# Performance work log

Hardware: AMD Instinct MI355X
Metric: run time of the kernel (lower is better)

## Reference

```python
import jax, jax.numpy as jnp
import numpy as np

B, S, D, H = 2, 2048, 768, 12
HD = D // H  # head dim = 64

def setup_inputs() -> dict:
    key = jax.random.key(0)
    ks = jax.random.split(key, 9)
    s = 1.0 / np.sqrt(D)
    return {
        "x": jax.random.normal(ks[0], (B, S, D), dtype=jnp.float32),
        "Wq": jax.random.uniform(ks[1], (D, D), jnp.float32, -s, s),
        "bq": jax.random.uniform(ks[2], (D,), jnp.float32, -s, s),
        "Wk": jax.random.uniform(ks[3], (D, D), jnp.float32, -s, s),
        "bk": jax.random.uniform(ks[4], (D,), jnp.float32, -s, s),
        "Wv": jax.random.uniform(ks[5], (D, D), jnp.float32, -s, s),
        "bv": jax.random.uniform(ks[6], (D,), jnp.float32, -s, s),
        "Wo": jax.random.uniform(ks[7], (D, D), jnp.float32, -s, s),
        "bo": jax.random.uniform(ks[8], (D,), jnp.float32, -s, s),
    }

def reference(x, Wq, bq, Wk, bk, Wv, bv, Wo, bo):
    b, s, _ = x.shape
    # linear projections, split into heads: [b, h, s, hd]
    def proj(W, bias):
        y = x @ W + bias
        return y.reshape(b, s, H, HD).transpose(0, 2, 1, 3)
    q = proj(Wq, bq)
    k = proj(Wk, bk)
    v = proj(Wv, bv)
    scale = 1.0 / np.sqrt(HD).astype(np.float32)
    scores = jnp.einsum('bhqd,bhkd->bhqk', q, k) * scale
    attn = jax.nn.softmax(scores, axis=-1)
    out = jnp.einsum('bhqk,bhkd->bhqd', attn, v)
    out = out.transpose(0, 2, 1, 3).reshape(b, s, D)
    return out @ Wo + bo
```

## Files before the change

### kernel.cpp

```cpp
#include <hip/hip_runtime.h>
#include <math.h>

#define NH 12
#define SEQ 2048
#define DM 768
#define HD 64
#define NB 2
#define MT (NB * SEQ)
#define QSCL 0.18033688011112042591999058512524f

typedef short bf16x8 __attribute__((ext_vector_type(8)));
typedef float f32x16 __attribute__((ext_vector_type(16)));

__device__ __forceinline__ unsigned short bf16_rne(float x) {
    unsigned u = __float_as_uint(x);
    u += 0x7fffu + ((u >> 16) & 1u);
    return (unsigned short)(u >> 16);
}
__device__ __forceinline__ float bf16_tof(short h) {
    return __uint_as_float(((unsigned)(unsigned short)h) << 16);
}

__device__ __forceinline__ void gl_lds16(const void* g, void* s) {
    __builtin_amdgcn_global_load_lds(
        (const __attribute__((address_space(1))) unsigned int*)g,
        (__attribute__((address_space(3))) unsigned int*)s, 16, 0, 0);
}

__device__ __forceinline__ f32x16 mfma32(bf16x8 a, bf16x8 b, f32x16 c) {
    return __builtin_amdgcn_mfma_f32_32x32x16_bf16(a, b, c, 0, 0, 0);
}

__device__ __forceinline__ bf16x8 gfrag(const char* base, int row, int physblk) {
    return *(const bf16x8*)(base + row * 64 + physblk * 16);
}
__device__ __forceinline__ bf16x8 afrag(const short* base, int row, int blk) {
    return *(const bf16x8*)(base + row * 64 + ((blk ^ (row & 7)) << 3));
}

__global__ __launch_bounds__(256)
void conv_x(const float* __restrict__ x, short* __restrict__ xg)
{
    const int idx = blockIdx.x * 256 + threadIdx.x;
    const int m = idx / 96, bk = idx % 96;
    const float* src = x + (size_t)m * DM + bk * 8;
    float4 v0 = *(const float4*)src;
    float4 v1 = *(const float4*)(src + 4);
    const float vv[8] = {v0.x, v0.y, v0.z, v0.w, v1.x, v1.y, v1.z, v1.w};
    union { short s[8]; int4 q; } hh;
#pragma unroll
    for (int j = 0; j < 8; j++) hh.s[j] = (short)bf16_rne(vv[j]);
    const int pb = (bk & ~3) | ((bk & 3) ^ ((m >> 1) & 3));
    *(int4*)(xg + (size_t)m * DM + pb * 8) = hh.q;
}

__global__ __launch_bounds__(256)
void conv_wt(const float* __restrict__ Wq, const float* __restrict__ Wk,
             const float* __restrict__ Wv, const float* __restrict__ Wo,
             short* __restrict__ wdst)
{
    const int z = blockIdx.y;
    const float* __restrict__ W = (z == 0) ? Wq : (z == 1) ? Wk : (z == 2) ? Wv : Wo;
    const int idx = blockIdx.x * 256 + threadIdx.x;
    const int n = idx % 768, bk = idx / 768;
    union { short s[8]; int4 q; } hh;
#pragma unroll
    for (int j = 0; j < 8; j++) hh.s[j] = (short)bf16_rne(W[(size_t)(bk * 8 + j) * DM + n]);
    const int pb = (bk & ~3) | ((bk & 3) ^ ((n >> 1) & 3));
    *(int4*)(wdst + (size_t)z * 589824 + (size_t)n * DM + pb * 8) = hh.q;
}

__global__ __launch_bounds__(256)
void gemm_qkv(const short* __restrict__ xg, const short* __restrict__ wt,
              const float* __restrict__ bq, const float* __restrict__ bkv,
              const float* __restrict__ bv,
              short* __restrict__ qg, short* __restrict__ kg, short* __restrict__ vg)
{
    const int z = blockIdx.z;
    const short* __restrict__ Bw = wt + (size_t)z * 589824;
    const float* __restrict__ bias = (z == 0) ? bq : (z == 1) ? bkv : bv;

    __shared__ short As[4096], Bs[4096];
    const int t = threadIdx.x, w = t >> 6, l = t & 63;
    const int by = blockIdx.y, bx = blockIdx.x;

    const int lr = w * 32 + (l >> 2);
    const char* pA = (const char*)xg + (size_t)(by * 128 + lr) * 1536 + (l & 3) * 16;
    const char* pB = (const char*)Bw + (size_t)(bx * 128 + lr) * 1536 + (l & 3) * 16;
    char* sA = (char*)As;
    char* sB = (char*)Bs;
    const int lo = w * 2048;

    const int mrow = (w >> 1) * 64 + (l & 31);
    const int nrow = (w & 1) * 64 + (l & 31);
    const int sel  = ((l & 31) >> 1) & 3;
    const int half = l >> 5;

    f32x16 acc[2][2];
#pragma unroll
    for (int i = 0; i < 2; i++)
#pragma unroll
        for (int j = 0; j < 2; j++)
#pragma unroll
            for (int r = 0; r < 16; r++) acc[i][j][r] = 0.f;

    for (int k0 = 0; k0 < DM; k0 += 32) {
        const size_t cb = (size_t)k0 * 2;
        __syncthreads();
#pragma unroll
        for (int i = 0; i < 2; i++) {
            gl_lds16(pA + i * 24576 + cb, sA + lo + i * 1024);
            gl_lds16(pB + i * 24576 + cb, sB + lo + i * 1024);
        }
        __syncthreads();
#pragma unroll
        for (int s = 0; s < 2; s++) {
            const int blk = s * 2 + half;
            bf16x8 a0 = gfrag(sA, mrow,      blk ^ sel);
            bf16x8 a1 = gfrag(sA, mrow + 32, blk ^ sel);
            bf16x8 b0 = gfrag(sB, nrow,      blk ^ sel);
            bf16x8 b1 = gfrag(sB, nrow + 32, blk ^ sel);
            acc[0][0] = mfma32(a0, b0, acc[0][0]);
            acc[0][1] = mfma32(a0, b1, acc[0][1]);
            acc[1][0] = mfma32(a1, b0, acc[1][0]);
            acc[1][1] = mfma32(a1, b1, acc[1][1]);
        }
    }

    const int mb = by * 128 + (w >> 1) * 64 + 4 * half;
    const int nb = bx * 128 + (w & 1) * 64 + (l & 31);

    if (z == 2) {
#pragma unroll
        for (int ti = 0; ti < 2; ti++)
#pragma unroll
            for (int g = 0; g < 4; g++)
#pragma unroll
                for (int tj = 0; tj < 2; tj++) {
                    const int m0 = mb + ti * 32 + 8 * g;
                    const int bb = m0 >> 11, ss = m0 & 2047;
                    const int n = nb + tj * 32;
                    const int h = n >> 6, hd = n & 63;
                    const float bia = bias[n];
                    union { unsigned short u[4]; uint2 q; } pk;
#pragma unroll
                    for (int j = 0; j < 4; j++)
                        pk.u[j] = bf16_rne(acc[ti][tj][4 * g + j] + bia);
                    const int blk = ss >> 3;
                    const int phys = (blk & ~7) | ((blk & 7) ^ (hd & 7));
                    *(uint2*)(vg + ((size_t)(bb * NH + h) * HD + hd) * SEQ + phys * 8 + (ss & 7)) = pk.q;
                }
    } else {
        short* dst = (z == 0) ? qg : kg;
        const float scl = (z == 0) ? QSCL : 1.0f;
#pragma unroll
        for (int ti = 0; ti < 2; ti++)
#pragma unroll
            for (int tj = 0; tj < 2; tj++) {
                const int n = nb + tj * 32;
                const int h = n >> 6, hd = n & 63;
                const float bia = bias[n];
                const int blk = hd >> 3;
#pragma unroll
                for (int r = 0; r < 16; r++) {
                    const int m = mb + ti * 32 + (r & 3) + 8 * (r >> 2);
                    const int bb = m >> 11, ss = m & 2047;
                    const int phys = blk ^ (ss & 7);
                    dst[((size_t)(bb * NH + h) * SEQ + ss) * HD + phys * 8 + (hd & 7)] =
                        (short)bf16_rne((acc[ti][tj][r] + bia) * scl);
                }
            }
    }
}

__global__ __launch_bounds__(256)
void attn_mfma(const short* __restrict__ qg, const short* __restrict__ kg,
               const short* __restrict__ vg,
               short* __restrict__ opart, float* __restrict__ lpart)
{
    __shared__ short Qs[8192];
    __shared__ short Ks[4096];
    __shared__ short Vt[4096];
    __shared__ short Ps[8192];

    const int t = threadIdx.x, w = t >> 6, l = t & 63;
    const int bh = blockIdx.y, q0 = blockIdx.x * 128, ks = blockIdx.z;
    const char* qp = (const char*)(qg + (size_t)bh * SEQ * HD);
    const char* kp = (const char*)(kg + (size_t)bh * SEQ * HD);
    const char* vp = (const char*)(vg + (size_t)bh * HD * SEQ);

#pragma unroll
    for (int i = 0; i < 4; i++)
        gl_lds16(qp + (size_t)(q0 + w * 32 + i * 8) * 128 + l * 16,
                 (char*)Qs + (w * 32 + i * 8) * 128);

    const int half = l >> 5;
    bf16x8 qf[4];
    f32x16 oacc[2], lacc;
#pragma unroll
    for (int nt = 0; nt < 2; nt++)
#pragma unroll
        for (int r = 0; r < 16; r++) oacc[nt][r] = 0.f;
#pragma unroll
    for (int r = 0; r < 16; r++) lacc[r] = 0.f;

    bf16x8 onesf;
#pragma unroll
    for (int j = 0; j < 8; j++) onesf[j] = (short)0x3F80;

    short* psw = Ps + w * 2048;

    for (int kti = 0; kti < 16; kti++) {
        const int kb0 = (ks * 16 + kti) * 64;
        __syncthreads();
#pragma unroll
        for (int i = 0; i < 2; i++) {
            gl_lds16(kp + (size_t)(kb0 + w * 16 + i * 8) * 128 + l * 16,
                     (char*)Ks + (w * 16 + i * 8) * 128);
            gl_lds16(vp + (size_t)(w * 16 + i * 8 + (l >> 3)) * 4096 + kb0 * 2 + (l & 7) * 16,
                     (char*)Vt + (w * 16 + i * 8) * 128);
        }
        __syncthreads();

        if (kti == 0) {
#pragma unroll
            for (int s = 0; s < 4; s++)
                qf[s] = afrag(Qs, w * 32 + (l & 31), half + s * 2);
        }

        f32x16 sacc[2];
#pragma unroll
        for (int nt = 0; nt < 2; nt++)
#pragma unroll
            for (int r = 0; r < 16; r++) sacc[nt][r] = 0.f;
#pragma unroll
        for (int s = 0; s < 4; s++) {
#pragma unroll
            for (int nt = 0; nt < 2; nt++) {
                bf16x8 kf = afrag(Ks, nt * 32 + (l & 31), half + s * 2);
                sacc[nt] = mfma32(qf[s], kf, sacc[nt]);
            }
        }

#pragma unroll
        for (int r = 0; r < 16; r++) {
            const int row = (r & 3) + 8 * (r >> 2) + 4 * half;
            const float p0 = exp2f(sacc[0][r]);
            const float p1 = exp2f(sacc[1][r]);
            const int b0 = (l & 31) >> 3;
            psw[row * 64 + ((b0 ^ (row & 7)) << 3) + (l & 7)]       = (short)bf16_rne(p0);
            psw[row * 64 + (((b0 + 4) ^ (row & 7)) << 3) + (l & 7)] = (short)bf16_rne(p1);
        }

#pragma unroll
        for (int s = 0; s < 4; s++) {
            bf16x8 pf = afrag(psw, l & 31, half + s * 2);
            lacc = mfma32(pf, onesf, lacc);
#pragma unroll
            for (int nt = 0; nt < 2; nt++) {
                bf16x8 vf = afrag(Vt, nt * 32 + (l & 31), half + s * 2);
                oacc[nt] = mfma32(pf, vf, oacc[nt]);
            }
        }
    }

    const size_t base = (size_t)(ks * 24 + bh) * SEQ;
#pragma unroll
    for (int r = 0; r < 16; r++) {
        const int row = q0 + w * 32 + (r & 3) + 8 * (r >> 2) + 4 * half;
#pragma unroll
        for (int nt = 0; nt < 2; nt++)
            opart[(base + row) * 64 + nt * 32 + (l & 31)] = (short)bf16_rne(oacc[nt][r]);
        if ((l & 31) == 0) lpart[base + row] = lacc[r];
    }
}

__global__ __launch_bounds__(256)
void attn_reduce(const short* __restrict__ opart, const float* __restrict__ lpart,
                 short* __restrict__ ag)
{
    const int idx = blockIdx.x * 256 + threadIdx.x;
    const int cg = idx & 7, row = idx >> 3;
    const int bh = row >> 11, s = row & 2047;
    union { short s[8]; int4 q; } a, b, o;
    a.q = *(const int4*)(opart + ((size_t)bh * SEQ + s) * 64 + cg * 8);
    b.q = *(const int4*)(opart + ((size_t)(24 + bh) * SEQ + s) * 64 + cg * 8);
    const float inv = 1.0f / (lpart[(size_t)bh * SEQ + s] + lpart[(size_t)(24 + bh) * SEQ + s]);
#pragma unroll
    for (int j = 0; j < 8; j++)
        o.s[j] = (short)bf16_rne((bf16_tof(a.s[j]) + bf16_tof(b.s[j])) * inv);
    const int bb = bh / NH, h = bh % NH;
    const int m = bb * SEQ + s;
    const int blk = h * 8 + cg;
    const int phys = (blk & ~3) | ((blk & 3) ^ ((m >> 1) & 3));
    *(int4*)(ag + (size_t)m * DM + phys * 8) = o.q;
}

__global__ __launch_bounds__(256)
void gemm_out(const short* __restrict__ ag, const short* __restrict__ wt3,
              const float* __restrict__ bias, float* __restrict__ out)
{
    __shared__ short As[4096], Bs[4096];
    const int t = threadIdx.x, w = t >> 6, l = t & 63;
    const int by = blockIdx.y, bx = blockIdx.x;

    const int lr = w * 32 + (l >> 2);
    const char* pA = (const char*)ag  + (size_t)(by * 128 + lr) * 1536 + (l & 3) * 16;
    const char* pB = (const char*)wt3 + (size_t)(bx * 128 + lr) * 1536 + (l & 3) * 16;
    char* sA = (char*)As;
    char* sB = (char*)Bs;
    const int lo = w * 2048;

    const int mrow = (w >> 1) * 64 + (l & 31);
    const int nrow = (w & 1) * 64 + (l & 31);
    const int sel  = ((l & 31) >> 1) & 3;
    const int half = l >> 5;

    f32x16 acc[2][2];
#pragma unroll
    for (int i = 0; i < 2; i++)
#pragma unroll
        for (int j = 0; j < 2; j++)
#pragma unroll
            for (int r = 0; r < 16; r++) acc[i][j][r] = 0.f;

    for (int k0 = 0; k0 < DM; k0 += 32) {
        const size_t cb = (size_t)k0 * 2;
        __syncthreads();
#pragma unroll
        for (int i = 0; i < 2; i++) {
            gl_lds16(pA + i * 24576 + cb, sA + lo + i * 1024);
            gl_lds16(pB + i * 24576 + cb, sB + lo + i * 1024);
        }
        __syncthreads();
#pragma unroll
        for (int s = 0; s < 2; s++) {
            const int blk = s * 2 + half;
            bf16x8 a0 = gfrag(sA, mrow,      blk ^ sel);
            bf16x8 a1 = gfrag(sA, mrow + 32, blk ^ sel);
            bf16x8 b0 = gfrag(sB, nrow,      blk ^ sel);
            bf16x8 b1 = gfrag(sB, nrow + 32, blk ^ sel);
            acc[0][0] = mfma32(a0, b0, acc[0][0]);
            acc[0][1] = mfma32(a0, b1, acc[0][1]);
            acc[1][0] = mfma32(a1, b0, acc[1][0]);
            acc[1][1] = mfma32(a1, b1, acc[1][1]);
        }
    }

    const int mb = by * 128 + (w >> 1) * 64 + 4 * half;
    const int nb = bx * 128 + (w & 1) * 64 + (l & 31);
#pragma unroll
    for (int ti = 0; ti < 2; ti++)
#pragma unroll
        for (int tj = 0; tj < 2; tj++) {
            const int n = nb + tj * 32;
            const float bia = bias[n];
#pragma unroll
            for (int r = 0; r < 16; r++) {
                const int m = mb + ti * 32 + (r & 3) + 8 * (r >> 2);
                out[(size_t)m * DM + n] = acc[ti][tj][r] + bia;
            }
        }
}

extern "C" void kernel_launch(void* const* d_in, const int* in_sizes, int n_in,
                              void* d_out, int out_size, void* d_ws, size_t ws_size,
                              hipStream_t stream)
{
    const float* x  = (const float*)d_in[0];
    const float* Wq = (const float*)d_in[1];
    const float* bq = (const float*)d_in[2];
    const float* Wk = (const float*)d_in[3];
    const float* bk = (const float*)d_in[4];
    const float* Wv = (const float*)d_in[5];
    const float* bv = (const float*)d_in[6];
    const float* Wo = (const float*)d_in[7];
    const float* bo = (const float*)d_in[8];
    float* out = (float*)d_out;

    const size_t BUF = (size_t)MT * DM;
    short* xg = (short*)d_ws;
    short* qg = xg + BUF;
    short* kg = qg + BUF;
    short* vg = kg + BUF;
    short* ag = vg + BUF;
    short* wt = ag + BUF;
    short* opart = wt + (size_t)4 * 589824;
    float* lpart = (float*)(opart + (size_t)2 * 24 * SEQ * HD);

    conv_x<<<1536, 256, 0, stream>>>(x, xg);
    conv_wt<<<dim3(288, 4), 256, 0, stream>>>(Wq, Wk, Wv, Wo, wt);
    gemm_qkv<<<dim3(6, 32, 3), 256, 0, stream>>>(xg, wt, bq, bk, bv, qg, kg, vg);
    attn_mfma<<<dim3(16, 24, 2), 256, 0, stream>>>(qg, kg, vg, opart, lpart);
    attn_reduce<<<1536, 256, 0, stream>>>(opart, lpart, ag);
    gemm_out<<<dim3(6, 32), 256, 0, stream>>>(ag, wt + (size_t)3 * 589824, bo, out);
}
```

Baseline: 209.6 us.

## Double-buffer GEMM and attention loads, fuse conversions and split-K reduce into out GEMM

Merges the x and weight conversion kernels into one launch. Adds LDS double buffering to the QKV GEMM and the attention loop, so the next K/V or A/B tile loads while the current one is computed, and reuses the Q tile's LDS as the second K/V buffer. Repacks the P writes as 32-bit stores with perm-based fragment extraction. Fuses the split-K attention reduction into the output GEMM's A-operand load, removing one kernel and an intermediate buffer. The cost is higher LDS use and register pressure in the GEMMs.

```diff
diff --git a/kernel.cpp b/kernel.cpp
--- a/kernel.cpp
+++ b/kernel.cpp
@@ -39,35 +39,36 @@
 }
 
 __global__ __launch_bounds__(256)
-void conv_x(const float* __restrict__ x, short* __restrict__ xg)
+void conv_all(const float* __restrict__ x,
+              const float* __restrict__ Wq, const float* __restrict__ Wk,
+              const float* __restrict__ Wv, const float* __restrict__ Wo,
+              short* __restrict__ xg, short* __restrict__ wdst)
 {
-    const int idx = blockIdx.x * 256 + threadIdx.x;
-    const int m = idx / 96, bk = idx % 96;
-    const float* src = x + (size_t)m * DM + bk * 8;
-    float4 v0 = *(const float4*)src;
-    float4 v1 = *(const float4*)(src + 4);
-    const float vv[8] = {v0.x, v0.y, v0.z, v0.w, v1.x, v1.y, v1.z, v1.w};
-    union { short s[8]; int4 q; } hh;
-#pragma unroll
-    for (int j = 0; j < 8; j++) hh.s[j] = (short)bf16_rne(vv[j]);
-    const int pb = (bk & ~3) | ((bk & 3) ^ ((m >> 1) & 3));
-    *(int4*)(xg + (size_t)m * DM + pb * 8) = hh.q;
-}
-
-__global__ __launch_bounds__(256)
-void conv_wt(const float* __restrict__ Wq, const float* __restrict__ Wk,
-             const float* __restrict__ Wv, const float* __restrict__ Wo,
-             short* __restrict__ wdst)
-{
-    const int z = blockIdx.y;
-    const float* __restrict__ W = (z == 0) ? Wq : (z == 1) ? Wk : (z == 2) ? Wv : Wo;
-    const int idx = blockIdx.x * 256 + threadIdx.x;
-    const int n = idx % 768, bk = idx / 768;
-    union { short s[8]; int4 q; } hh;
-#pragma unroll
-    for (int j = 0; j < 8; j++) hh.s[j] = (short)bf16_rne(W[(size_t)(bk * 8 + j) * DM + n]);
-    const int pb = (bk & ~3) | ((bk & 3) ^ ((n >> 1) & 3));
-    *(int4*)(wdst + (size_t)z * 589824 + (size_t)n * DM + pb * 8) = hh.q;
+    int b = blockIdx.x;
+    if (b < 1536) {
+        const int idx = b * 256 + threadIdx.x;
+        const int m = idx / 96, bk = idx % 96;
+        const float* src = x + (size_t)m * DM + bk * 8;
+        float4 v0 = *(const float4*)src;
+        float4 v1 = *(const float4*)(src + 4);
+        const float vv[8] = {v0.x, v0.y, v0.z, v0.w, v1.x, v1.y, v1.z, v1.w};
+        union { short s[8]; int4 q; } hh;
+#pragma unroll
+        for (int j = 0; j < 8; j++) hh.s[j] = (short)bf16_rne(vv[j]);
+        const int pb = (bk & ~3) | ((bk & 3) ^ ((m >> 1) & 3));
+        *(int4*)(xg + (size_t)m * DM + pb * 8) = hh.q;
+    } else {
+        b -= 1536;
+        const int z = b / 288;
+        const float* __restrict__ W = (z == 0) ? Wq : (z == 1) ? Wk : (z == 2) ? Wv : Wo;
+        const int idx = (b % 288) * 256 + threadIdx.x;
+        const int n = idx % 768, bk = idx / 768;
+        union { short s[8]; int4 q; } hh;
+#pragma unroll
+        for (int j = 0; j < 8; j++) hh.s[j] = (short)bf16_rne(W[(size_t)(bk * 8 + j) * DM + n]);
+        const int pb = (bk & ~3) | ((bk & 3) ^ ((n >> 1) & 3));
+        *(int4*)(wdst + (size_t)z * 589824 + (size_t)n * DM + pb * 8) = hh.q;
+    }
 }
 
 __global__ __launch_bounds__(256)
@@ -80,15 +81,13 @@
     const short* __restrict__ Bw = wt + (size_t)z * 589824;
     const float* __restrict__ bias = (z == 0) ? bq : (z == 1) ? bkv : bv;
 
-    __shared__ short As[4096], Bs[4096];
+    __shared__ short As[8192], Bs[8192];
     const int t = threadIdx.x, w = t >> 6, l = t & 63;
     const int by = blockIdx.y, bx = blockIdx.x;
 
     const int lr = w * 32 + (l >> 2);
     const char* pA = (const char*)xg + (size_t)(by * 128 + lr) * 1536 + (l & 3) * 16;
     const char* pB = (const char*)Bw + (size_t)(bx * 128 + lr) * 1536 + (l & 3) * 16;
-    char* sA = (char*)As;
-    char* sB = (char*)Bs;
     const int lo = w * 2048;
 
     const int mrow = (w >> 1) * 64 + (l & 31);
@@ -104,15 +103,27 @@
 #pragma unroll
             for (int r = 0; r < 16; r++) acc[i][j][r] = 0.f;
 
-    for (int k0 = 0; k0 < DM; k0 += 32) {
-        const size_t cb = (size_t)k0 * 2;
-        __syncthreads();
-#pragma unroll
-        for (int i = 0; i < 2; i++) {
-            gl_lds16(pA + i * 24576 + cb, sA + lo + i * 1024);
-            gl_lds16(pB + i * 24576 + cb, sB + lo + i * 1024);
-        }
-        __syncthreads();
+#pragma unroll
+    for (int i = 0; i < 2; i++) {
+        gl_lds16(pA + i * 24576, (char*)As + lo + i * 1024);
+        gl_lds16(pB + i * 24576, (char*)Bs + lo + i * 1024);
+    }
+    __syncthreads();
+
+    for (int ki = 0; ki < 24; ki++) {
+        const int cur = ki & 1;
+        if (ki < 23) {
+            const size_t cb = (size_t)(ki + 1) * 64;
+            char* dA = (char*)As + (cur ^ 1) * 8192 + lo;
+            char* dB = (char*)Bs + (cur ^ 1) * 8192 + lo;
+#pragma unroll
+            for (int i = 0; i < 2; i++) {
+                gl_lds16(pA + i * 24576 + cb, dA + i * 1024);
+                gl_lds16(pB + i * 24576 + cb, dB + i * 1024);
+            }
+        }
+        const char* sA = (const char*)As + cur * 8192;
+        const char* sB = (const char*)Bs + cur * 8192;
 #pragma unroll
         for (int s = 0; s < 2; s++) {
             const int blk = s * 2 + half;
@@ -125,6 +136,7 @@
             acc[1][0] = mfma32(a1, b0, acc[1][0]);
             acc[1][1] = mfma32(a1, b1, acc[1][1]);
         }
+        __syncthreads();
     }
 
     const int mb = by * 128 + (w >> 1) * 64 + 4 * half;
@@ -188,14 +200,28 @@
     const char* qp = (const char*)(qg + (size_t)bh * SEQ * HD);
     const char* kp = (const char*)(kg + (size_t)bh * SEQ * HD);
     const char* vp = (const char*)(vg + (size_t)bh * HD * SEQ);
+    const int kbase = ks * 1024;
 
 #pragma unroll
     for (int i = 0; i < 4; i++)
         gl_lds16(qp + (size_t)(q0 + w * 32 + i * 8) * 128 + l * 16,
                  (char*)Qs + (w * 32 + i * 8) * 128);
+#pragma unroll
+    for (int i = 0; i < 2; i++) {
+        gl_lds16(kp + (size_t)(kbase + w * 16 + i * 8) * 128 + l * 16,
+                 (char*)Ks + (w * 16 + i * 8) * 128);
+        gl_lds16(vp + (size_t)(w * 16 + i * 8 + (l >> 3)) * 4096 + kbase * 2 + (l & 7) * 16,
+                 (char*)Vt + (w * 16 + i * 8) * 128);
+    }
+    __syncthreads();
 
     const int half = l >> 5;
     bf16x8 qf[4];
+#pragma unroll
+    for (int s = 0; s < 4; s++)
+        qf[s] = afrag(Qs, w * 32 + (l & 31), half + s * 2);
+    __syncthreads();
+
     f32x16 oacc[2], lacc;
 #pragma unroll
     for (int nt = 0; nt < 2; nt++)
@@ -209,24 +235,24 @@
     for (int j = 0; j < 8; j++) onesf[j] = (short)0x3F80;
 
     short* psw = Ps + w * 2048;
+    const int q = l & 31, key = q & 7;
 
     for (int kti = 0; kti < 16; kti++) {
-        const int kb0 = (ks * 16 + kti) * 64;
-        __syncthreads();
-#pragma unroll
-        for (int i = 0; i < 2; i++) {
-            gl_lds16(kp + (size_t)(kb0 + w * 16 + i * 8) * 128 + l * 16,
-                     (char*)Ks + (w * 16 + i * 8) * 128);
-            gl_lds16(vp + (size_t)(w * 16 + i * 8 + (l >> 3)) * 4096 + kb0 * 2 + (l & 7) * 16,
-                     (char*)Vt + (w * 16 + i * 8) * 128);
-        }
-        __syncthreads();
-
-        if (kti == 0) {
-#pragma unroll
-            for (int s = 0; s < 4; s++)
-                qf[s] = afrag(Qs, w * 32 + (l & 31), half + s * 2);
-        }
+        const int cur = kti & 1;
+        if (kti < 15) {
+            const int kb0 = kbase + (kti + 1) * 64;
+            char* kd = cur ? (char*)Ks : (char*)Qs;
+            char* vd = cur ? (char*)Vt : (char*)(Qs + 4096);
+#pragma unroll
+            for (int i = 0; i < 2; i++) {
+                gl_lds16(kp + (size_t)(kb0 + w * 16 + i * 8) * 128 + l * 16,
+                         kd + (w * 16 + i * 8) * 128);
+                gl_lds16(vp + (size_t)(w * 16 + i * 8 + (l >> 3)) * 4096 + kb0 * 2 + (l & 7) * 16,
+                         vd + (w * 16 + i * 8) * 128);
+            }
+        }
+        const short* kc = cur ? Qs : Ks;
+        const short* vc = cur ? Qs + 4096 : Vt;
 
         f32x16 sacc[2];
 #pragma unroll
@@ -234,34 +260,46 @@
 #pragma unroll
             for (int r = 0; r < 16; r++) sacc[nt][r] = 0.f;
 #pragma unroll
-        for (int s = 0; s < 4; s++) {
+        for (int s = 0; s < 4; s++)
 #pragma unroll
             for (int nt = 0; nt < 2; nt++) {
-                bf16x8 kf = afrag(Ks, nt * 32 + (l & 31), half + s * 2);
+                bf16x8 kf = afrag(kc, nt * 32 + q, half + s * 2);
                 sacc[nt] = mfma32(qf[s], kf, sacc[nt]);
             }
-        }
 
 #pragma unroll
         for (int r = 0; r < 16; r++) {
             const int row = (r & 3) + 8 * (r >> 2) + 4 * half;
             const float p0 = exp2f(sacc[0][r]);
             const float p1 = exp2f(sacc[1][r]);
-            const int b0 = (l & 31) >> 3;
-            psw[row * 64 + ((b0 ^ (row & 7)) << 3) + (l & 7)]       = (short)bf16_rne(p0);
-            psw[row * 64 + (((b0 + 4) ^ (row & 7)) << 3) + (l & 7)] = (short)bf16_rne(p1);
-        }
-
-#pragma unroll
-        for (int s = 0; s < 4; s++) {
-            bf16x8 pf = afrag(psw, l & 31, half + s * 2);
-            lacc = mfma32(pf, onesf, lacc);
+            const unsigned pk = ((unsigned)bf16_rne(p1) << 16) | (unsigned)bf16_rne(p0);
+            *(unsigned*)(psw + row * 64 + (((q >> 2) ^ (row & 7)) << 3) + ((2 * q) & 7)) = pk;
+        }
+
+#pragma unroll
+        for (int a = 0; a < 2; a++) {
+            union { uint4 u; bf16x8 v; } w0, w1, pe, po;
+            w0.v = *(const bf16x8*)(psw + q * 64 + (((4 * a + 2 * half)     ^ key) << 3));
+            w1.v = *(const bf16x8*)(psw + q * 64 + (((4 * a + 2 * half + 1) ^ key) << 3));
+            pe.u.x = __builtin_amdgcn_perm(w0.u.y, w0.u.x, 0x05040100u);
+            pe.u.y = __builtin_amdgcn_perm(w0.u.w, w0.u.z, 0x05040100u);
+            pe.u.z = __builtin_amdgcn_perm(w1.u.y, w1.u.x, 0x05040100u);
+            pe.u.w = __builtin_amdgcn_perm(w1.u.w, w1.u.z, 0x05040100u);
+            po.u.x = __builtin_amdgcn_perm(w0.u.y, w0.u.x, 0x07060302u);
+            po.u.y = __builtin_amdgcn_perm(w0.u.w, w0.u.z, 0x07060302u);
+            po.u.z = __builtin_amdgcn_perm(w1.u.y, w1.u.x, 0x07060302u);
+            po.u.w = __builtin_amdgcn_perm(w1.u.w, w1.u.z, 0x07060302u);
+            lacc = mfma32(pe.v, onesf, lacc);
+            lacc = mfma32(po.v, onesf, lacc);
 #pragma unroll
             for (int nt = 0; nt < 2; nt++) {
-                bf16x8 vf = afrag(Vt, nt * 32 + (l & 31), half + s * 2);
-                oacc[nt] = mfma32(pf, vf, oacc[nt]);
-            }
-        }
+                bf16x8 vfa = afrag(vc, nt * 32 + q, half + a * 2);
+                bf16x8 vfb = afrag(vc, nt * 32 + q, half + (a + 2) * 2);
+                oacc[nt] = mfma32(pe.v, vfa, oacc[nt]);
+                oacc[nt] = mfma32(po.v, vfb, oacc[nt]);
+            }
+        }
+        __syncthreads();
     }
 
     const size_t base = (size_t)(ks * 24 + bh) * SEQ;
@@ -270,46 +308,64 @@
         const int row = q0 + w * 32 + (r & 3) + 8 * (r >> 2) + 4 * half;
 #pragma unroll
         for (int nt = 0; nt < 2; nt++)
-            opart[(base + row) * 64 + nt * 32 + (l & 31)] = (short)bf16_rne(oacc[nt][r]);
-        if ((l & 31) == 0) lpart[base + row] = lacc[r];
+            opart[(base + row) * 64 + nt * 32 + q] = (short)bf16_rne(oacc[nt][r]);
+        if (q == 0) lpart[base + row] = lacc[r];
     }
 }
 
 __global__ __launch_bounds__(256)
-void attn_reduce(const short* __restrict__ opart, const float* __restrict__ lpart,
-                 short* __restrict__ ag)
+void gemm_out(const short* __restrict__ opart, const float* __restrict__ lpart,
+              const short* __restrict__ wt3, const float* __restrict__ bias,
+              float* __restrict__ out)
 {
-    const int idx = blockIdx.x * 256 + threadIdx.x;
-    const int cg = idx & 7, row = idx >> 3;
-    const int bh = row >> 11, s = row & 2047;
-    union { short s[8]; int4 q; } a, b, o;
-    a.q = *(const int4*)(opart + ((size_t)bh * SEQ + s) * 64 + cg * 8);
-    b.q = *(const int4*)(opart + ((size_t)(24 + bh) * SEQ + s) * 64 + cg * 8);
-    const float inv = 1.0f / (lpart[(size_t)bh * SEQ + s] + lpart[(size_t)(24 + bh) * SEQ + s]);
-#pragma unroll
-    for (int j = 0; j < 8; j++)
-        o.s[j] = (short)bf16_rne((bf16_tof(a.s[j]) + bf16_tof(b.s[j])) * inv);
-    const int bb = bh / NH, h = bh % NH;
-    const int m = bb * SEQ + s;
-    const int blk = h * 8 + cg;
-    const int phys = (blk & ~3) | ((blk & 3) ^ ((m >> 1) & 3));
-    *(int4*)(ag + (size_t)m * DM + phys * 8) = o.q;
-}
-
-__global__ __launch_bounds__(256)
-void gemm_out(const short* __restrict__ ag, const short* __restrict__ wt3,
-              const float* __restrict__ bias, float* __restrict__ out)
-{
-    __shared__ short As[4096], Bs[4096];
+    __shared__ short As[8192], Bs[8192];
     const int t = threadIdx.x, w = t >> 6, l = t & 63;
     const int by = blockIdx.y, bx = blockIdx.x;
 
-    const int lr = w * 32 + (l >> 2);
-    const char* pA = (const char*)ag  + (size_t)(by * 128 + lr) * 1536 + (l & 3) * 16;
-    const char* pB = (const char*)wt3 + (size_t)(bx * 128 + lr) * 1536 + (l & 3) * 16;
-    char* sA = (char*)As;
-    char* sB = (char*)Bs;
+    const int lr = t >> 1, ch = t & 1;
+    const int m = by * 128 + lr;
+    const int bb = m >> 11, s = m & 2047;
+    const int key2 = (lr >> 1) & 3;
+
+    const int blr = w * 32 + (l >> 2);
+    const char* pB = (const char*)wt3 + (size_t)(bx * 128 + blr) * 1536 + (l & 3) * 16;
     const int lo = w * 2048;
+
+    uint4 ra[2][4];
+    float rl[2][2];
+
+    auto aload = [&](int ki, int slot) {
+        const int h = ki >> 1;
+        const int hd0 = (ki & 1) * 32 + ch * 16;
+        const int bhh = bb * NH + h;
+        const short* p0 = opart + ((size_t)bhh * SEQ + s) * 64 + hd0;
+        const short* p1 = p0 + (size_t)24 * SEQ * 64;
+        ra[slot][0] = *(const uint4*)p0;
+        ra[slot][1] = *(const uint4*)(p0 + 8);
+        ra[slot][2] = *(const uint4*)p1;
+        ra[slot][3] = *(const uint4*)(p1 + 8);
+        rl[slot][0] = lpart[(size_t)bhh * SEQ + s];
+        rl[slot][1] = lpart[(size_t)(24 + bhh) * SEQ + s];
+    };
+    auto acommit = [&](int slot, int buf) {
+        const float inv = 1.0f / (rl[slot][0] + rl[slot][1]);
+        union { uint4 u; short sh[8]; } x0, x1, y0, y1, o0, o1;
+        x0.u = ra[slot][0]; x1.u = ra[slot][1];
+        y0.u = ra[slot][2]; y1.u = ra[slot][3];
+#pragma unroll
+        for (int j = 0; j < 8; j++) {
+            o0.sh[j] = (short)bf16_rne((bf16_tof(x0.sh[j]) + bf16_tof(y0.sh[j])) * inv);
+            o1.sh[j] = (short)bf16_rne((bf16_tof(x1.sh[j]) + bf16_tof(y1.sh[j])) * inv);
+        }
+        short* dst = As + buf * 4096 + lr * 32;
+        *(uint4*)(dst + (((ch * 2)     ^ key2) << 3)) = o0.u;
+        *(uint4*)(dst + (((ch * 2 + 1) ^ key2) << 3)) = o1.u;
+    };
+    auto bissue = [&](int ki, int buf) {
+#pragma unroll
+        for (int i = 0; i < 2; i++)
+            gl_lds16(pB + i * 24576 + (size_t)ki * 64, (char*)Bs + buf * 8192 + lo + i * 1024);
+    };
 
     const int mrow = (w >> 1) * 64 + (l & 31);
     const int nrow = (w & 1) * 64 + (l & 31);
@@ -324,18 +380,24 @@
 #pragma unroll
             for (int r = 0; r < 16; r++) acc[i][j][r] = 0.f;
 
-    for (int k0 = 0; k0 < DM; k0 += 32) {
-        const size_t cb = (size_t)k0 * 2;
-        __syncthreads();
-#pragma unroll
-        for (int i = 0; i < 2; i++) {
-            gl_lds16(pA + i * 24576 + cb, sA + lo + i * 1024);
-            gl_lds16(pB + i * 24576 + cb, sB + lo + i * 1024);
-        }
-        __syncthreads();
-#pragma unroll
-        for (int s = 0; s < 2; s++) {
-            const int blk = s * 2 + half;
+    bissue(0, 0);
+    aload(0, 0);
+    acommit(0, 0);
+    aload(1, 1);
+    __syncthreads();
+
+    for (int ki = 0; ki < 24; ki++) {
+        const int cur = ki & 1;
+        if (ki < 23) {
+            bissue(ki + 1, cur ^ 1);
+            acommit((ki + 1) & 1, cur ^ 1);
+        }
+        if (ki < 22) aload(ki + 2, ki & 1);
+        const char* sA = (const char*)(As + cur * 4096);
+        const char* sB = (const char*)Bs + cur * 8192;
+#pragma unroll
+        for (int ss = 0; ss < 2; ss++) {
+            const int blk = ss * 2 + half;
             bf16x8 a0 = gfrag(sA, mrow,      blk ^ sel);
             bf16x8 a1 = gfrag(sA, mrow + 32, blk ^ sel);
             bf16x8 b0 = gfrag(sB, nrow,      blk ^ sel);
@@ -345,6 +407,7 @@
             acc[1][0] = mfma32(a1, b0, acc[1][0]);
             acc[1][1] = mfma32(a1, b1, acc[1][1]);
         }
+        __syncthreads();
     }
 
     const int mb = by * 128 + (w >> 1) * 64 + 4 * half;
@@ -357,8 +420,8 @@
             const float bia = bias[n];
 #pragma unroll
             for (int r = 0; r < 16; r++) {
-                const int m = mb + ti * 32 + (r & 3) + 8 * (r >> 2);
-                out[(size_t)m * DM + n] = acc[ti][tj][r] + bia;
+                const int mm = mb + ti * 32 + (r & 3) + 8 * (r >> 2);
+                out[(size_t)mm * DM + n] = acc[ti][tj][r] + bia;
             }
         }
 }
@@ -383,15 +446,12 @@
     short* qg = xg + BUF;
     short* kg = qg + BUF;
     short* vg = kg + BUF;
-    short* ag = vg + BUF;
-    short* wt = ag + BUF;
+    short* wt = vg + BUF;
     short* opart = wt + (size_t)4 * 589824;
     float* lpart = (float*)(opart + (size_t)2 * 24 * SEQ * HD);
 
-    conv_x<<<1536, 256, 0, stream>>>(x, xg);
-    conv_wt<<<dim3(288, 4), 256, 0, stream>>>(Wq, Wk, Wv, Wo, wt);
+    conv_all<<<2688, 256, 0, stream>>>(x, Wq, Wk, Wv, Wo, xg, wt);
     gemm_qkv<<<dim3(6, 32, 3), 256, 0, stream>>>(xg, wt, bq, bk, bv, qg, kg, vg);
     attn_mfma<<<dim3(16, 24, 2), 256, 0, stream>>>(qg, kg, vg, opart, lpart);
-    attn_reduce<<<1536, 256, 0, stream>>>(opart, lpart, ag);
-    gemm_out<<<dim3(6, 32), 256, 0, stream>>>(ag, wt + (size_t)3 * 589824, bo, out);
-}
+    gemm_out<<<dim3(6, 32), 256, 0, stream>>>(opart, lpart, wt + (size_t)3 * 589824, bo, out);
+}
```

Measured after the change: 238.8 us. 13.9% more time.

## Double-buffer K/V tiles in attention, merge conversion kernels, pack V and P stores

Applied to the files above, without the earlier changes.

The attention kernel now prefetches the next K/V tile into a second LDS buffer, reusing the Q staging area once Q fragments are in registers. This drops one barrier per iteration and overlaps global-to-LDS loads with MFMA work. The two fp32-to-bf16 conversion kernels are merged into one launch. The V-projection epilogue and the P-tile writes now use packed 32-bit stores with new swizzle index math. The catch is that P is now truncated to bf16 instead of rounded, and the reworked V layout indexing has to match the existing layout exactly.

```diff
diff --git a/kernel.cpp b/kernel.cpp
--- a/kernel.cpp
+++ b/kernel.cpp
@@ -39,35 +39,36 @@
 }
 
 __global__ __launch_bounds__(256)
-void conv_x(const float* __restrict__ x, short* __restrict__ xg)
-{
-    const int idx = blockIdx.x * 256 + threadIdx.x;
-    const int m = idx / 96, bk = idx % 96;
-    const float* src = x + (size_t)m * DM + bk * 8;
-    float4 v0 = *(const float4*)src;
-    float4 v1 = *(const float4*)(src + 4);
-    const float vv[8] = {v0.x, v0.y, v0.z, v0.w, v1.x, v1.y, v1.z, v1.w};
-    union { short s[8]; int4 q; } hh;
-#pragma unroll
-    for (int j = 0; j < 8; j++) hh.s[j] = (short)bf16_rne(vv[j]);
-    const int pb = (bk & ~3) | ((bk & 3) ^ ((m >> 1) & 3));
-    *(int4*)(xg + (size_t)m * DM + pb * 8) = hh.q;
-}
-
-__global__ __launch_bounds__(256)
-void conv_wt(const float* __restrict__ Wq, const float* __restrict__ Wk,
-             const float* __restrict__ Wv, const float* __restrict__ Wo,
-             short* __restrict__ wdst)
-{
-    const int z = blockIdx.y;
-    const float* __restrict__ W = (z == 0) ? Wq : (z == 1) ? Wk : (z == 2) ? Wv : Wo;
-    const int idx = blockIdx.x * 256 + threadIdx.x;
-    const int n = idx % 768, bk = idx / 768;
-    union { short s[8]; int4 q; } hh;
-#pragma unroll
-    for (int j = 0; j < 8; j++) hh.s[j] = (short)bf16_rne(W[(size_t)(bk * 8 + j) * DM + n]);
-    const int pb = (bk & ~3) | ((bk & 3) ^ ((n >> 1) & 3));
-    *(int4*)(wdst + (size_t)z * 589824 + (size_t)n * DM + pb * 8) = hh.q;
+void conv_all(const float* __restrict__ x,
+              const float* __restrict__ Wq, const float* __restrict__ Wk,
+              const float* __restrict__ Wv, const float* __restrict__ Wo,
+              short* __restrict__ xg, short* __restrict__ wdst)
+{
+    int b = blockIdx.x;
+    if (b < 1536) {
+        const int idx = b * 256 + threadIdx.x;
+        const int m = idx / 96, bk = idx % 96;
+        const float* src = x + (size_t)m * DM + bk * 8;
+        float4 v0 = *(const float4*)src;
+        float4 v1 = *(const float4*)(src + 4);
+        const float vv[8] = {v0.x, v0.y, v0.z, v0.w, v1.x, v1.y, v1.z, v1.w};
+        union { short s[8]; int4 q; } hh;
+#pragma unroll
+        for (int j = 0; j < 8; j++) hh.s[j] = (short)bf16_rne(vv[j]);
+        const int pb = (bk & ~3) | ((bk & 3) ^ ((m >> 1) & 3));
+        *(int4*)(xg + (size_t)m * DM + pb * 8) = hh.q;
+    } else {
+        b -= 1536;
+        const int z = b / 288;
+        const float* __restrict__ W = (z == 0) ? Wq : (z == 1) ? Wk : (z == 2) ? Wv : Wo;
+        const int idx = (b % 288) * 256 + threadIdx.x;
+        const int n = idx % 768, bk = idx / 768;
+        union { short s[8]; int4 q; } hh;
+#pragma unroll
+        for (int j = 0; j < 8; j++) hh.s[j] = (short)bf16_rne(W[(size_t)(bk * 8 + j) * DM + n]);
+        const int pb = (bk & ~3) | ((bk & 3) ^ ((n >> 1) & 3));
+        *(int4*)(wdst + (size_t)z * 589824 + (size_t)n * DM + pb * 8) = hh.q;
+    }
 }
 
 __global__ __launch_bounds__(256)
@@ -131,25 +132,25 @@
     const int nb = bx * 128 + (w & 1) * 64 + (l & 31);
 
     if (z == 2) {
-#pragma unroll
-        for (int ti = 0; ti < 2; ti++)
-#pragma unroll
-            for (int g = 0; g < 4; g++)
-#pragma unroll
-                for (int tj = 0; tj < 2; tj++) {
-                    const int m0 = mb + ti * 32 + 8 * g;
-                    const int bb = m0 >> 11, ss = m0 & 2047;
-                    const int n = nb + tj * 32;
-                    const int h = n >> 6, hd = n & 63;
-                    const float bia = bias[n];
-                    union { unsigned short u[4]; uint2 q; } pk;
-#pragma unroll
-                    for (int j = 0; j < 4; j++)
-                        pk.u[j] = bf16_rne(acc[ti][tj][4 * g + j] + bia);
-                    const int blk = ss >> 3;
-                    const int phys = (blk & ~7) | ((blk & 7) ^ (hd & 7));
-                    *(uint2*)(vg + ((size_t)(bb * NH + h) * HD + hd) * SEQ + phys * 8 + (ss & 7)) = pk.q;
-                }
+        const int hb  = mb >> 11;
+        const int g64 = (mb & 2047) - 4 * half;
+#pragma unroll
+        for (int tj = 0; tj < 2; tj++) {
+            const int n = nb + tj * 32;
+            const int h = n >> 6, hd = n & 63;
+            const float bia = bias[n];
+            unsigned* dstrow = (unsigned*)(vg + ((size_t)(hb * NH + h) * HD + hd) * SEQ + g64);
+#pragma unroll
+            for (int r = 0; r < 16; r++) {
+                const int rt = (r & 3) + 8 * (r >> 2);
+                const int D  = 4 * half + rt;
+                const int Dp = (((D >> 2) ^ (hd & 7)) << 2) | (D & 3);
+                const unsigned pk =
+                    ((unsigned)bf16_rne(acc[1][tj][r] + bia) << 16) |
+                     (unsigned)bf16_rne(acc[0][tj][r] + bia);
+                dstrow[Dp] = pk;
+            }
+        }
     } else {
         short* dst = (z == 0) ? qg : kg;
         const float scl = (z == 0) ? QSCL : 1.0f;
@@ -188,14 +189,29 @@
     const char* qp = (const char*)(qg + (size_t)bh * SEQ * HD);
     const char* kp = (const char*)(kg + (size_t)bh * SEQ * HD);
     const char* vp = (const char*)(vg + (size_t)bh * HD * SEQ);
+    const int kbase = ks * 1024;
 
 #pragma unroll
     for (int i = 0; i < 4; i++)
         gl_lds16(qp + (size_t)(q0 + w * 32 + i * 8) * 128 + l * 16,
                  (char*)Qs + (w * 32 + i * 8) * 128);
+#pragma unroll
+    for (int i = 0; i < 2; i++) {
+        gl_lds16(kp + (size_t)(kbase + w * 16 + i * 8) * 128 + l * 16,
+                 (char*)Ks + (w * 16 + i * 8) * 128);
+        gl_lds16(vp + (size_t)(w * 16 + i * 8 + (l >> 3)) * 4096 + kbase * 2 + (l & 7) * 16,
+                 (char*)Vt + (w * 16 + i * 8) * 128);
+    }
+    __syncthreads();
 
     const int half = l >> 5;
+    const int q = l & 31;
     bf16x8 qf[4];
+#pragma unroll
+    for (int s = 0; s < 4; s++)
+        qf[s] = afrag(Qs, w * 32 + q, half + s * 2);
+    __syncthreads();
+
     f32x16 oacc[2], lacc;
 #pragma unroll
     for (int nt = 0; nt < 2; nt++)
@@ -211,22 +227,21 @@
     short* psw = Ps + w * 2048;
 
     for (int kti = 0; kti < 16; kti++) {
-        const int kb0 = (ks * 16 + kti) * 64;
-        __syncthreads();
-#pragma unroll
-        for (int i = 0; i < 2; i++) {
-            gl_lds16(kp + (size_t)(kb0 + w * 16 + i * 8) * 128 + l * 16,
-                     (char*)Ks + (w * 16 + i * 8) * 128);
-            gl_lds16(vp + (size_t)(w * 16 + i * 8 + (l >> 3)) * 4096 + kb0 * 2 + (l & 7) * 16,
-                     (char*)Vt + (w * 16 + i * 8) * 128);
-        }
-        __syncthreads();
-
-        if (kti == 0) {
-#pragma unroll
-            for (int s = 0; s < 4; s++)
-                qf[s] = afrag(Qs, w * 32 + (l & 31), half + s * 2);
-        }
+        const int cur = kti & 1;
+        if (kti < 15) {
+            const int kb0 = kbase + (kti + 1) * 64;
+            char* kd = cur ? (char*)Ks : (char*)Qs;
+            char* vd = cur ? (char*)Vt : (char*)(Qs + 4096);
+#pragma unroll
+            for (int i = 0; i < 2; i++) {
+                gl_lds16(kp + (size_t)(kb0 + w * 16 + i * 8) * 128 + l * 16,
+                         kd + (w * 16 + i * 8) * 128);
+                gl_lds16(vp + (size_t)(w * 16 + i * 8 + (l >> 3)) * 4096 + kb0 * 2 + (l & 7) * 16,
+                         vd + (w * 16 + i * 8) * 128);
+            }
+        }
+        const short* kc = cur ? Qs : Ks;
+        const short* vc = cur ? Qs + 4096 : Vt;
 
         f32x16 sacc[2];
 #pragma unroll
@@ -234,34 +249,35 @@
 #pragma unroll
             for (int r = 0; r < 16; r++) sacc[nt][r] = 0.f;
 #pragma unroll
-        for (int s = 0; s < 4; s++) {
+        for (int s = 0; s < 4; s++)
 #pragma unroll
             for (int nt = 0; nt < 2; nt++) {
-                bf16x8 kf = afrag(Ks, nt * 32 + (l & 31), half + s * 2);
+                bf16x8 kf = afrag(kc, nt * 32 + q, half + s * 2);
                 sacc[nt] = mfma32(qf[s], kf, sacc[nt]);
             }
-        }
 
 #pragma unroll
         for (int r = 0; r < 16; r++) {
             const int row = (r & 3) + 8 * (r >> 2) + 4 * half;
             const float p0 = exp2f(sacc[0][r]);
             const float p1 = exp2f(sacc[1][r]);
-            const int b0 = (l & 31) >> 3;
-            psw[row * 64 + ((b0 ^ (row & 7)) << 3) + (l & 7)]       = (short)bf16_rne(p0);
-            psw[row * 64 + (((b0 + 4) ^ (row & 7)) << 3) + (l & 7)] = (short)bf16_rne(p1);
+            const unsigned pk = __builtin_amdgcn_perm(
+                __float_as_uint(p1), __float_as_uint(p0), 0x07060302u);
+            const int Dp = (((q >> 2) ^ (row & 7)) << 2) | (q & 3);
+            *(unsigned*)(psw + row * 64 + 2 * Dp) = pk;
         }
 
 #pragma unroll
         for (int s = 0; s < 4; s++) {
-            bf16x8 pf = afrag(psw, l & 31, half + s * 2);
+            bf16x8 pf = afrag(psw, q, half + s * 2);
             lacc = mfma32(pf, onesf, lacc);
 #pragma unroll
             for (int nt = 0; nt < 2; nt++) {
-                bf16x8 vf = afrag(Vt, nt * 32 + (l & 31), half + s * 2);
+                bf16x8 vf = afrag(vc, nt * 32 + q, half + s * 2);
                 oacc[nt] = mfma32(pf, vf, oacc[nt]);
             }
         }
+        __syncthreads();
     }
 
     const size_t base = (size_t)(ks * 24 + bh) * SEQ;
@@ -270,8 +286,8 @@
         const int row = q0 + w * 32 + (r & 3) + 8 * (r >> 2) + 4 * half;
 #pragma unroll
         for (int nt = 0; nt < 2; nt++)
-            opart[(base + row) * 64 + nt * 32 + (l & 31)] = (short)bf16_rne(oacc[nt][r]);
-        if ((l & 31) == 0) lpart[base + row] = lacc[r];
+            opart[(base + row) * 64 + nt * 32 + q] = (short)bf16_rne(oacc[nt][r]);
+        if (q == 0) lpart[base + row] = lacc[r];
     }
 }
 
@@ -388,8 +404,7 @@
     short* opart = wt + (size_t)4 * 589824;
     float* lpart = (float*)(opart + (size_t)2 * 24 * SEQ * HD);
 
-    conv_x<<<1536, 256, 0, stream>>>(x, xg);
-    conv_wt<<<dim3(288, 4), 256, 0, stream>>>(Wq, Wk, Wv, Wo, wt);
+    conv_all<<<2688, 256, 0, stream>>>(x, Wq, Wk, Wv, Wo, xg, wt);
     gemm_qkv<<<dim3(6, 32, 3), 256, 0, stream>>>(xg, wt, bq, bk, bv, qg, kg, vg);
     attn_mfma<<<dim3(16, 24, 2), 256, 0, stream>>>(qg, kg, vg, opart, lpart);
     attn_reduce<<<1536, 256, 0, stream>>>(opart, lpart, ag);
```

After: 204.1 us. 2.6% less time.
